# Optimization experiments

Hardware: AMD Instinct MI355X
Metric: run time of the kernel (lower is better)

The kernel has to match this reference:

```python
import jax, jax.numpy as jnp
import numpy as np

N_GRAPHS = 64

def setup_inputs() -> dict:
    key = jax.random.key(0)
    ks = jax.random.split(key, 8)
    N, E, H = 50000, 600000, 128
    x = jax.random.normal(ks[0], (N, 2), dtype=jnp.float32)
    edge_index = jax.random.randint(ks[1], (2, E), 0, N, dtype=jnp.int64)
    batch = jnp.sort(jax.random.randint(ks[2], (N,), 0, N_GRAPHS, dtype=jnp.int64))
    s = 0.1  # keep tanh out of saturation
    return {
        'x': x,
        'edge_index': edge_index,
        'batch': batch,
        'W1': jax.random.normal(ks[3], (2, H), dtype=jnp.float32) * s,
        'b1': jnp.zeros((H,), jnp.float32),
        'W2': jax.random.normal(ks[4], (H, H), dtype=jnp.float32) * s,
        'b2': jnp.zeros((H,), jnp.float32),
        'W3': jax.random.normal(ks[5], (H, H), dtype=jnp.float32) * s,
        'b3': jnp.zeros((H,), jnp.float32),
        'Wo': jax.random.normal(ks[6], (2 * H, 41), dtype=jnp.float32) * s,
        'bo': jnp.zeros((41,), jnp.float32),
    }

def reference(x, edge_index, batch, W1, b1, W2, b2, W3, b3, Wo, bo):
    N = x.shape[0]
    src, dst = edge_index[0], edge_index[1]
    # GCN symmetric normalization with self loops: deg = in-degree + 1
    ones_e = jnp.ones(src.shape[0], dtype=x.dtype)
    deg = jax.ops.segment_sum(ones_e, dst, num_segments=N) + 1.0
    dinv = jax.lax.rsqrt(deg)                       # [N]
    edge_norm = (dinv[src] * dinv[dst])[:, None]    # [E,1]
    self_norm = (dinv * dinv)[:, None]              # [N,1]

    def gcn(h, W, b):
        h = h @ W                                   # [N,H] transform first
        agg = jax.ops.segment_sum(h[src] * edge_norm, dst, num_segments=N)
        return agg + h * self_norm + b

    h = jnp.tanh(gcn(x, W1, b1))
    h = jnp.tanh(gcn(h, W2, b2))
    h = jnp.tanh(gcn(h, W3, b3))

    # global max pool + global mean pool over graphs
    cnt = jax.ops.segment_sum(jnp.ones(N, dtype=h.dtype), batch, num_segments=N_GRAPHS)
    mx = jax.ops.segment_max(h, batch, num_segments=N_GRAPHS)
    mx = jnp.where(cnt[:, None] > 0, mx, 0.0)
    mean = jax.ops.segment_sum(h, batch, num_segments=N_GRAPHS) / jnp.maximum(cnt, 1.0)[:, None]
    pooled = jnp.concatenate([mx, mean], axis=1)    # [G, 2H]
    return jnp.tanh(pooled @ Wo + bo)               # [G, 41]
```

## Files before the change

### kernel.cpp

```cpp
#include <hip/hip_runtime.h>
#include <math.h>

#define NGRAPH 64
#define POOL_CHUNKS 32
#define SCAN_BLK 1024

typedef short short8 __attribute__((ext_vector_type(8)));
typedef float floatx4 __attribute__((ext_vector_type(4)));

__device__ inline unsigned pack_bf16x2(float a, float b) {
    unsigned ua = __float_as_uint(a);
    unsigned ub = __float_as_uint(b);
    ua = (ua + 0x7fffu + ((ua >> 16) & 1u)) >> 16;
    ub = (ub + 0x7fffu + ((ub >> 16) & 1u)) >> 16;
    return ua | (ub << 16);
}
__device__ inline unsigned short bf16_1(float a) {
    unsigned ua = __float_as_uint(a);
    return (unsigned short)((ua + 0x7fffu + ((ua >> 16) & 1u)) >> 16);
}
__device__ inline float bf16lo(unsigned u) { return __uint_as_float(u << 16); }
__device__ inline float bf16hi(unsigned u) { return __uint_as_float(u & 0xffff0000u); }



__global__ void pack_count(const int* __restrict__ dst, int E, int* __restrict__ cnt,
                           const float* __restrict__ W2, const float* __restrict__ W3,
                           unsigned* __restrict__ Wt2, unsigned* __restrict__ Wt3) {
    if (blockIdx.x < 32) {
        int b = blockIdx.x;
        const float* W = (b < 16) ? W2 : W3;
        unsigned* Wt = (b < 16) ? Wt2 : Wt3;
        b &= 15;
        int bk = b & 3, bn = b >> 2;
        __shared__ float s[32][33];
        int tx = threadIdx.x & 31, ty = threadIdx.x >> 5;
#pragma unroll
        for (int r = 0; r < 4; ++r)
            s[r * 8 + ty][tx] = W[(bk * 32 + r * 8 + ty) * 128 + bn * 32 + tx];
        __syncthreads();
        int t16 = threadIdx.x & 15, tn = threadIdx.x >> 4;
#pragma unroll
        for (int pass = 0; pass < 2; ++pass) {
            int nl = pass * 16 + tn;
            unsigned pk = pack_bf16x2(s[2 * t16][nl], s[2 * t16 + 1][nl]);
            Wt[(bn * 32 + nl) * 64 + bk * 16 + t16] = pk;
        }
    } else {
        int e = (blockIdx.x - 32) * blockDim.x + threadIdx.x;
        if (e < E) atomicAdd(&cnt[dst[e]], 1);
    }
}


__global__ __launch_bounds__(SCAN_BLK) void scan_phase1(const int* __restrict__ cnt,
                                                        const float* __restrict__ x,
                                                        int* __restrict__ row_ptr,
                                                        int* __restrict__ bsum,
                                                        float* __restrict__ dinv,
                                                        float2* __restrict__ y, int N) {
    __shared__ int sm[SCAN_BLK];
    int i = blockIdx.x * SCAN_BLK + threadIdx.x;
    int v = (i < N) ? cnt[i] : 0;
    if (i < N) {
        float dv = rsqrtf((float)v + 1.0f);
        dinv[i] = dv;
        float2 xv = ((const float2*)x)[i];
        y[i] = make_float2(xv.x * dv, xv.y * dv);
    }
    sm[threadIdx.x] = v;
    __syncthreads();
    for (int off = 1; off < SCAN_BLK; off <<= 1) {
        int t = (threadIdx.x >= (unsigned)off) ? sm[threadIdx.x - off] : 0;
        __syncthreads();
        sm[threadIdx.x] += t;
        __syncthreads();
    }
    if (i < N) row_ptr[i] = sm[threadIdx.x] - v;
    if (threadIdx.x == SCAN_BLK - 1) bsum[blockIdx.x] = sm[SCAN_BLK - 1];
}

__global__ __launch_bounds__(SCAN_BLK) void scan_phase2(int* __restrict__ bsum, int nb,
                                                        const int* __restrict__ batch, int N,
                                                        int* __restrict__ goff) {
    if (threadIdx.x <= NGRAPH) {
        int g = threadIdx.x;
        int lo = 0, hi = N;
        while (lo < hi) {
            int mid = (lo + hi) >> 1;
            if (batch[mid] < g) lo = mid + 1; else hi = mid;
        }
        goff[g] = lo;
    }
    __shared__ int sm[SCAN_BLK];
    int v = (threadIdx.x < (unsigned)nb) ? bsum[threadIdx.x] : 0;
    sm[threadIdx.x] = v;
    __syncthreads();
    for (int off = 1; off < SCAN_BLK; off <<= 1) {
        int t = (threadIdx.x >= (unsigned)off) ? sm[threadIdx.x - off] : 0;
        __syncthreads();
        sm[threadIdx.x] += t;
        __syncthreads();
    }
    if (threadIdx.x < (unsigned)nb) bsum[threadIdx.x] = sm[threadIdx.x] - v;
}

__global__ __launch_bounds__(SCAN_BLK) void scan_phase3(int* __restrict__ row_ptr,
                                                        const int* __restrict__ bsum,
                                                        int N, int E) {
    int i = blockIdx.x * SCAN_BLK + threadIdx.x;
    if (i < N) row_ptr[i] += bsum[blockIdx.x];
    if (i == 0) row_ptr[N] = E;
}

__global__ void fill_kernel(const int* __restrict__ src, const int* __restrict__ dst, int E,
                            const int* __restrict__ row_ptr, int* __restrict__ cnt,
                            int* __restrict__ col) {
    int e = blockIdx.x * blockDim.x + threadIdx.x;
    if (e < E) {
        int d = dst[e];
        int p = row_ptr[d] + atomicSub(&cnt[d], 1) - 1;
        col[p] = src[e];
    }
}


__global__ __launch_bounds__(256) void agg_x_t1(const float2* __restrict__ y,
                                                const int* __restrict__ row_ptr,
                                                const int* __restrict__ col,
                                                const float* __restrict__ dinv,
                                                const float* __restrict__ W1,
                                                const float* __restrict__ b1,
                                                unsigned short* __restrict__ h, int N) {
    __shared__ float4 sW[64];
    __shared__ float4 sb[32];
    __shared__ float2 zs[256];
    if (threadIdx.x < 64) sW[threadIdx.x] = ((const float4*)W1)[threadIdx.x];
    if (threadIdx.x < 32) sb[threadIdx.x] = ((const float4*)b1)[threadIdx.x];

    int v = blockIdx.x * 256 + threadIdx.x;
    float2 zv = make_float2(0.f, 0.f);
    if (v < N) {
        int s = row_ptr[v], e = row_ptr[v + 1];
        float2 a0 = y[v];
        float2 a1 = make_float2(0.f, 0.f);
        float2 a2 = make_float2(0.f, 0.f);
        float2 a3 = make_float2(0.f, 0.f);
        int j = s;
        for (; j + 4 <= e; j += 4) {
            int u0 = col[j], u1 = col[j + 1], u2 = col[j + 2], u3 = col[j + 3];
            float2 v0 = y[u0], v1 = y[u1], v2 = y[u2], v3 = y[u3];
            a0.x += v0.x; a0.y += v0.y;
            a1.x += v1.x; a1.y += v1.y;
            a2.x += v2.x; a2.y += v2.y;
            a3.x += v3.x; a3.y += v3.y;
        }
        for (; j < e; ++j) {
            float2 vv = y[col[j]];
            a0.x += vv.x; a0.y += vv.y;
        }
        float dv = dinv[v];
        zv = make_float2(dv * (a0.x + a1.x + a2.x + a3.x),
                         dv * (a0.y + a1.y + a2.y + a3.y));
    }
    zs[threadIdx.x] = zv;
    __syncthreads();

    int q = threadIdx.x & 31;
    int rsub = threadIdx.x >> 5;
    float4 w0 = sW[q];
    float4 w1 = sW[32 + q];
    float4 b = sb[q];
    size_t qoff = (size_t)(q >> 3) * N;
#pragma unroll 4
    for (int pass = 0; pass < 32; ++pass) {
        int local = pass * 8 + rsub;
        int row = blockIdx.x * 256 + local;
        if (row >= N) break;
        float2 z = zs[local];
        float ox = tanhf(fmaf(z.x, w0.x, fmaf(z.y, w1.x, b.x)));
        float oy = tanhf(fmaf(z.x, w0.y, fmaf(z.y, w1.y, b.y)));
        float oz = tanhf(fmaf(z.x, w0.z, fmaf(z.y, w1.z, b.z)));
        float ow = tanhf(fmaf(z.x, w0.w, fmaf(z.y, w1.w, b.w)));
        uint2 pk;
        pk.x = pack_bf16x2(ox, oy);
        pk.y = pack_bf16x2(oz, ow);
        ((uint2*)h)[(qoff + row) * 8 + (q & 7)] = pk;
    }
}


__global__ __launch_bounds__(256) void gemm_mfma(const unsigned short* __restrict__ A,
                                                 const unsigned* __restrict__ Wt,
                                                 const float* __restrict__ dinv,
                                                 unsigned short* __restrict__ t, int N) {
    __shared__ unsigned sW[128 * 68];
    const uint4* Wt4 = (const uint4*)Wt;
    for (int i = threadIdx.x; i < 2048; i += 256) {
        int n = i >> 4, c = i & 15;
        *(uint4*)&sW[n * 68 + c * 4] = Wt4[i];
    }
    __syncthreads();
    int w = threadIdx.x >> 6;
    int l = threadIdx.x & 63;
    int lm = l & 15;
    int q4 = l >> 4;
    int k8 = q4 * 8;

    floatx4 acc[2][8];
#pragma unroll
    for (int i = 0; i < 2; ++i)
#pragma unroll
        for (int j = 0; j < 8; ++j) acc[i][j] = (floatx4){0.f, 0.f, 0.f, 0.f};

    int rowbase = blockIdx.x * 128 + w * 32;
#pragma unroll
    for (int ks = 0; ks < 4; ++ks) {
        short8 a[2];
#pragma unroll
        for (int mt = 0; mt < 2; ++mt) {
            int r = min(rowbase + mt * 16 + lm, N - 1);
            a[mt] = *(const short8*)(A + ((size_t)ks * N + r) * 32 + k8);
        }
#pragma unroll
        for (int nt = 0; nt < 8; ++nt) {
            short8 b = *(const short8*)&sW[(nt * 16 + lm) * 68 + ks * 16 + q4 * 4];
#pragma unroll
            for (int mt = 0; mt < 2; ++mt)
                acc[mt][nt] = __builtin_amdgcn_mfma_f32_16x16x32_bf16(a[mt], b, acc[mt][nt], 0, 0, 0);
        }
    }

#pragma unroll
    for (int mt = 0; mt < 2; ++mt) {
#pragma unroll
        for (int reg = 0; reg < 4; ++reg) {
            int gr = rowbase + mt * 16 + q4 * 4 + reg;
            if (gr >= N) continue;
            float dv = dinv[gr];
#pragma unroll
            for (int nt = 0; nt < 8; ++nt) {
                t[((size_t)(nt >> 1) * N + gr) * 32 + (nt & 1) * 16 + lm] =
                    bf16_1(acc[mt][nt][reg] * dv);
            }
        }
    }
}


__global__ __launch_bounds__(256) void agg_kernel(const unsigned short* __restrict__ t,
                                                  const int* __restrict__ row_ptr,
                                                  const int* __restrict__ col,
                                                  const float* __restrict__ dinv,
                                                  const float* __restrict__ bias,
                                                  unsigned short* __restrict__ out, int N) {
    int lane = threadIdx.x & 63;
    int wave = threadIdx.x >> 6;
    int grp = lane >> 2;
    int q = lane & 3;
    int qt = blockIdx.y;
    int node = blockIdx.x * 64 + wave * 16 + grp;
    if (node >= N) return;
    const uint4* t4 = (const uint4*)t;
    unsigned qb = (unsigned)qt * (unsigned)N;
    int s = row_ptr[node];
    int deg = row_ptr[node + 1] - s;

    float a[8];
    {
        uint4 v = t4[(size_t)((qb + (unsigned)node) * 4u + q)];
        a[0] = bf16lo(v.x); a[1] = bf16hi(v.x);
        a[2] = bf16lo(v.y); a[3] = bf16hi(v.y);
        a[4] = bf16lo(v.z); a[5] = bf16hi(v.z);
        a[6] = bf16lo(v.w); a[7] = bf16hi(v.w);
    }
    int j = 0;
    for (; j + 4 <= deg; j += 4) {
        int u0 = col[s + j];
        int u1 = col[s + j + 1];
        int u2 = col[s + j + 2];
        int u3 = col[s + j + 3];
        uint4 v0 = t4[(size_t)((qb + (unsigned)u0) * 4u + q)];
        uint4 v1 = t4[(size_t)((qb + (unsigned)u1) * 4u + q)];
        uint4 v2 = t4[(size_t)((qb + (unsigned)u2) * 4u + q)];
        uint4 v3 = t4[(size_t)((qb + (unsigned)u3) * 4u + q)];
        a[0] += bf16lo(v0.x); a[1] += bf16hi(v0.x);
        a[2] += bf16lo(v0.y); a[3] += bf16hi(v0.y);
        a[4] += bf16lo(v0.z); a[5] += bf16hi(v0.z);
        a[6] += bf16lo(v0.w); a[7] += bf16hi(v0.w);
        a[0] += bf16lo(v1.x); a[1] += bf16hi(v1.x);
        a[2] += bf16lo(v1.y); a[3] += bf16hi(v1.y);
        a[4] += bf16lo(v1.z); a[5] += bf16hi(v1.z);
        a[6] += bf16lo(v1.w); a[7] += bf16hi(v1.w);
        a[0] += bf16lo(v2.x); a[1] += bf16hi(v2.x);
        a[2] += bf16lo(v2.y); a[3] += bf16hi(v2.y);
        a[4] += bf16lo(v2.z); a[5] += bf16hi(v2.z);
        a[6] += bf16lo(v2.w); a[7] += bf16hi(v2.w);
        a[0] += bf16lo(v3.x); a[1] += bf16hi(v3.x);
        a[2] += bf16lo(v3.y); a[3] += bf16hi(v3.y);
        a[4] += bf16lo(v3.z); a[5] += bf16hi(v3.z);
        a[6] += bf16lo(v3.w); a[7] += bf16hi(v3.w);
    }
    for (; j < deg; ++j) {
        int u = col[s + j];
        uint4 v = t4[(size_t)((qb + (unsigned)u) * 4u + q)];
        a[0] += bf16lo(v.x); a[1] += bf16hi(v.x);
        a[2] += bf16lo(v.y); a[3] += bf16hi(v.y);
        a[4] += bf16lo(v.z); a[5] += bf16hi(v.z);
        a[6] += bf16lo(v.w); a[7] += bf16hi(v.w);
    }

    float dv = dinv[node];
    const float4* b4 = (const float4*)bias;
    float4 b0 = b4[qt * 8 + q * 2];
    float4 b1 = b4[qt * 8 + q * 2 + 1];
    uint4 pk;
    pk.x = pack_bf16x2(tanhf(fmaf(dv, a[0], b0.x)), tanhf(fmaf(dv, a[1], b0.y)));
    pk.y = pack_bf16x2(tanhf(fmaf(dv, a[2], b0.z)), tanhf(fmaf(dv, a[3], b0.w)));
    pk.z = pack_bf16x2(tanhf(fmaf(dv, a[4], b1.x)), tanhf(fmaf(dv, a[5], b1.y)));
    pk.w = pack_bf16x2(tanhf(fmaf(dv, a[6], b1.z)), tanhf(fmaf(dv, a[7], b1.w)));
    ((uint4*)out)[(size_t)((qb + (unsigned)node) * 4u + q)] = pk;
}


__global__ __launch_bounds__(128) void pool_partial(const unsigned short* __restrict__ h,
                                                    const int* __restrict__ goff,
                                                    float* __restrict__ part, int N) {
    int g = blockIdx.x;
    int c = blockIdx.y;
    int j = threadIdx.x;
    int s = goff[g], e = goff[g + 1];
    int cnt = e - s;
    int per = (cnt + POOL_CHUNKS - 1) / POOL_CHUNKS;
    int ps = s + c * per;
    int pe = min(ps + per, e);
    size_t qoff = (size_t)(j >> 5) * N;
    int jq = j & 31;
    float mx = -3.402823466e+38f, sm = 0.f;
    for (int n = ps; n < pe; ++n) {
        float v = __uint_as_float(((unsigned)h[(qoff + n) * 32 + jq]) << 16);
        mx = fmaxf(mx, v);
        sm += v;
    }
    float* dst = part + ((size_t)g * POOL_CHUNKS + c) * 256;
    dst[j] = mx;
    dst[128 + j] = sm;
}

__global__ __launch_bounds__(128) void pool_final(const float* __restrict__ part,
                                                  const int* __restrict__ goff,
                                                  const float* __restrict__ Wo,
                                                  const float* __restrict__ bo,
                                                  float* __restrict__ out) {
    __shared__ float p[256];
    int g = blockIdx.x;
    int j = threadIdx.x;
    float mx = -3.402823466e+38f, sm = 0.f;
    const float* base = part + (size_t)g * POOL_CHUNKS * 256;
#pragma unroll 4
    for (int c = 0; c < POOL_CHUNKS; ++c) {
        mx = fmaxf(mx, base[c * 256 + j]);
        sm += base[c * 256 + 128 + j];
    }
    int cnt = goff[g + 1] - goff[g];
    p[j] = (cnt > 0) ? mx : 0.f;
    p[128 + j] = sm / fmaxf((float)cnt, 1.f);
    __syncthreads();
    if (j < 41) {
        float acc = bo[j];
        for (int k = 0; k < 256; ++k) acc = fmaf(p[k], Wo[k * 41 + j], acc);
        out[g * 41 + j] = tanhf(acc);
    }
}


extern "C" void kernel_launch(void* const* d_in, const int* in_sizes, int n_in,
                              void* d_out, int out_size, void* d_ws, size_t ws_size,
                              hipStream_t stream) {
    const float* x   = (const float*)d_in[0];
    const int*   ei  = (const int*)d_in[1];
    const int* batch = (const int*)d_in[2];
    const float* W1  = (const float*)d_in[3];
    const float* b1  = (const float*)d_in[4];
    const float* W2  = (const float*)d_in[5];
    const float* b2  = (const float*)d_in[6];
    const float* W3  = (const float*)d_in[7];
    const float* b3  = (const float*)d_in[8];
    const float* Wo  = (const float*)d_in[9];
    const float* bo  = (const float*)d_in[10];
    float* outp = (float*)d_out;

    int N = in_sizes[2];
    int E = in_sizes[1] / 2;
    const int* src = ei;
    const int* dst = ei + E;

    char* p = (char*)d_ws;
    auto alloc = [&](size_t bytes) -> char* {
        char* q = p;
        p += (bytes + 255) & ~(size_t)255;
        return q;
    };
    unsigned short* t   = (unsigned short*)alloc((size_t)N * 128 * 2);
    unsigned short* hb  = (unsigned short*)alloc((size_t)N * 128 * 2);
    unsigned short* h3b = (unsigned short*)alloc((size_t)N * 128 * 2);
    float* dinv   = (float*)alloc((size_t)N * 4);
    int*   cnt    = (int*)alloc((size_t)N * 4);
    int*   rowp   = (int*)alloc((size_t)(N + 1) * 4);
    int*   col    = (int*)alloc((size_t)E * 4);
    int*   goff   = (int*)alloc(65 * 4);
    float* part   = (float*)alloc((size_t)NGRAPH * POOL_CHUNKS * 256 * 4);
    float2* y     = (float2*)alloc((size_t)N * 8);
    unsigned* Wt2 = (unsigned*)alloc(128 * 64 * 4);
    unsigned* Wt3 = (unsigned*)alloc(128 * 64 * 4);
    int nscan = (N + SCAN_BLK - 1) / SCAN_BLK;
    int*   bsum   = (int*)alloc((size_t)nscan * 4);

    hipMemsetAsync(cnt, 0, (size_t)N * 4, stream);

    pack_count<<<32 + (E + 255) / 256, 256, 0, stream>>>(dst, E, cnt, W2, W3, Wt2, Wt3);
    scan_phase1<<<nscan, SCAN_BLK, 0, stream>>>(cnt, x, rowp, bsum, dinv, y, N);
    scan_phase2<<<1, SCAN_BLK, 0, stream>>>(bsum, nscan, batch, N, goff);
    scan_phase3<<<nscan, SCAN_BLK, 0, stream>>>(rowp, bsum, N, E);
    fill_kernel<<<(E + 255) / 256, 256, 0, stream>>>(src, dst, E, rowp, cnt, col);

    dim3 agrid((N + 63) / 64, 4);

    agg_x_t1<<<(N + 255) / 256, 256, 0, stream>>>(y, rowp, col, dinv, W1, b1, hb, N);
    gemm_mfma<<<(N + 127) / 128, 256, 0, stream>>>(hb, Wt2, dinv, t, N);
    agg_kernel<<<agrid, 256, 0, stream>>>(t, rowp, col, dinv, b2, hb, N);
    gemm_mfma<<<(N + 127) / 128, 256, 0, stream>>>(hb, Wt3, dinv, t, N);
    agg_kernel<<<agrid, 256, 0, stream>>>(t, rowp, col, dinv, b3, h3b, N);

    dim3 pgrid(NGRAPH, POOL_CHUNKS);
    pool_partial<<<pgrid, 128, 0, stream>>>(h3b, goff, part, N);
    pool_final<<<NGRAPH, 128, 0, stream>>>(part, goff, Wo, bo, outp);
}
```

Baseline: 277.9 us.

## Fuse scan phases via last-block ticket and fuse pooling into final aggregation

```diff
diff --git a/kernel.cpp b/kernel.cpp
--- a/kernel.cpp
+++ b/kernel.cpp
@@ -2,7 +2,6 @@
 #include <math.h>
 
 #define NGRAPH 64
-#define POOL_CHUNKS 32
 #define SCAN_BLK 1024
 
 typedef short short8 __attribute__((ext_vector_type(8)));
@@ -21,6 +20,11 @@
 }
 __device__ inline float bf16lo(unsigned u) { return __uint_as_float(u << 16); }
 __device__ inline float bf16hi(unsigned u) { return __uint_as_float(u & 0xffff0000u); }
+
+__device__ inline unsigned fkey(float v) {
+    unsigned u = __float_as_uint(v);
+    return (v >= 0.f) ? (u | 0x80000000u) : ~u;
+}
 
 
 
@@ -53,13 +57,17 @@
 }
 
 
-__global__ __launch_bounds__(SCAN_BLK) void scan_phase1(const int* __restrict__ cnt,
-                                                        const float* __restrict__ x,
-                                                        int* __restrict__ row_ptr,
-                                                        int* __restrict__ bsum,
-                                                        float* __restrict__ dinv,
-                                                        float2* __restrict__ y, int N) {
+__global__ __launch_bounds__(SCAN_BLK) void scanA(const int* __restrict__ cnt,
+                                                  const float* __restrict__ x,
+                                                  int* __restrict__ row_ptr,
+                                                  int* __restrict__ bsum,
+                                                  float* __restrict__ dinv,
+                                                  float2* __restrict__ y,
+                                                  const int* __restrict__ batch,
+                                                  int* __restrict__ ticket,
+                                                  int* __restrict__ goff, int N) {
     __shared__ int sm[SCAN_BLK];
+    __shared__ int amLast;
     int i = blockIdx.x * SCAN_BLK + threadIdx.x;
     int v = (i < N) ? cnt[i] : 0;
     if (i < N) {
@@ -78,11 +86,24 @@
     }
     if (i < N) row_ptr[i] = sm[threadIdx.x] - v;
     if (threadIdx.x == SCAN_BLK - 1) bsum[blockIdx.x] = sm[SCAN_BLK - 1];
-}
-
-__global__ __launch_bounds__(SCAN_BLK) void scan_phase2(int* __restrict__ bsum, int nb,
-                                                        const int* __restrict__ batch, int N,
-                                                        int* __restrict__ goff) {
+    __syncthreads();
+    if (threadIdx.x == 0) {
+        __threadfence();
+        amLast = (atomicAdd(ticket, 1) == (int)gridDim.x - 1);
+    }
+    __syncthreads();
+    if (!amLast) return;
+    int nb = (int)gridDim.x;
+    int v2 = (threadIdx.x < (unsigned)nb) ? atomicAdd(&bsum[threadIdx.x], 0) : 0;
+    sm[threadIdx.x] = v2;
+    __syncthreads();
+    for (int off = 1; off < SCAN_BLK; off <<= 1) {
+        int t = (threadIdx.x >= (unsigned)off) ? sm[threadIdx.x - off] : 0;
+        __syncthreads();
+        sm[threadIdx.x] += t;
+        __syncthreads();
+    }
+    if (threadIdx.x < (unsigned)nb) bsum[threadIdx.x] = sm[threadIdx.x] - v2;
     if (threadIdx.x <= NGRAPH) {
         int g = threadIdx.x;
         int lo = 0, hi = N;
@@ -92,34 +113,16 @@
         }
         goff[g] = lo;
     }
-    __shared__ int sm[SCAN_BLK];
-    int v = (threadIdx.x < (unsigned)nb) ? bsum[threadIdx.x] : 0;
-    sm[threadIdx.x] = v;
-    __syncthreads();
-    for (int off = 1; off < SCAN_BLK; off <<= 1) {
-        int t = (threadIdx.x >= (unsigned)off) ? sm[threadIdx.x - off] : 0;
-        __syncthreads();
-        sm[threadIdx.x] += t;
-        __syncthreads();
-    }
-    if (threadIdx.x < (unsigned)nb) bsum[threadIdx.x] = sm[threadIdx.x] - v;
-}
-
-__global__ __launch_bounds__(SCAN_BLK) void scan_phase3(int* __restrict__ row_ptr,
-                                                        const int* __restrict__ bsum,
-                                                        int N, int E) {
-    int i = blockIdx.x * SCAN_BLK + threadIdx.x;
-    if (i < N) row_ptr[i] += bsum[blockIdx.x];
-    if (i == 0) row_ptr[N] = E;
 }
 
 __global__ void fill_kernel(const int* __restrict__ src, const int* __restrict__ dst, int E,
-                            const int* __restrict__ row_ptr, int* __restrict__ cnt,
-                            int* __restrict__ col) {
+                            const int* __restrict__ row_ptr, const int* __restrict__ bsum,
+                            int* __restrict__ cnt, int* __restrict__ col) {
     int e = blockIdx.x * blockDim.x + threadIdx.x;
     if (e < E) {
         int d = dst[e];
-        int p = row_ptr[d] + atomicSub(&cnt[d], 1) - 1;
+        int base = row_ptr[d] + bsum[d >> 10];
+        int p = base + atomicSub(&cnt[d], 1) - 1;
         col[p] = src[e];
     }
 }
@@ -127,11 +130,12 @@
 
 __global__ __launch_bounds__(256) void agg_x_t1(const float2* __restrict__ y,
                                                 const int* __restrict__ row_ptr,
+                                                const int* __restrict__ bsum,
                                                 const int* __restrict__ col,
                                                 const float* __restrict__ dinv,
                                                 const float* __restrict__ W1,
                                                 const float* __restrict__ b1,
-                                                unsigned short* __restrict__ h, int N) {
+                                                unsigned short* __restrict__ h, int N, int E) {
     __shared__ float4 sW[64];
     __shared__ float4 sb[32];
     __shared__ float2 zs[256];
@@ -141,7 +145,8 @@
     int v = blockIdx.x * 256 + threadIdx.x;
     float2 zv = make_float2(0.f, 0.f);
     if (v < N) {
-        int s = row_ptr[v], e = row_ptr[v + 1];
+        int s = row_ptr[v] + bsum[v >> 10];
+        int e = (v + 1 < N) ? row_ptr[v + 1] + bsum[(v + 1) >> 10] : E;
         float2 a0 = y[v];
         float2 a1 = make_float2(0.f, 0.f);
         float2 a2 = make_float2(0.f, 0.f);
@@ -248,23 +253,22 @@
 }
 
 
-__global__ __launch_bounds__(256) void agg_kernel(const unsigned short* __restrict__ t,
-                                                  const int* __restrict__ row_ptr,
-                                                  const int* __restrict__ col,
-                                                  const float* __restrict__ dinv,
-                                                  const float* __restrict__ bias,
-                                                  unsigned short* __restrict__ out, int N) {
-    int lane = threadIdx.x & 63;
-    int wave = threadIdx.x >> 6;
-    int grp = lane >> 2;
-    int q = lane & 3;
+__global__ __launch_bounds__(1024) void agg_kernel(const unsigned short* __restrict__ t,
+                                                   const int* __restrict__ row_ptr,
+                                                   const int* __restrict__ bsum,
+                                                   const int* __restrict__ col,
+                                                   const float* __restrict__ dinv,
+                                                   const float* __restrict__ bias,
+                                                   unsigned short* __restrict__ out, int N, int E) {
+    int q = threadIdx.x & 3;
+    int node = blockIdx.x * 256 + (threadIdx.x >> 2);
     int qt = blockIdx.y;
-    int node = blockIdx.x * 64 + wave * 16 + grp;
     if (node >= N) return;
     const uint4* t4 = (const uint4*)t;
     unsigned qb = (unsigned)qt * (unsigned)N;
-    int s = row_ptr[node];
-    int deg = row_ptr[node + 1] - s;
+    int s = row_ptr[node] + bsum[node >> 10];
+    int e = (node + 1 < N) ? row_ptr[node + 1] + bsum[(node + 1) >> 10] : E;
+    int deg = e - s;
 
     float a[8];
     {
@@ -323,31 +327,158 @@
 }
 
 
-__global__ __launch_bounds__(128) void pool_partial(const unsigned short* __restrict__ h,
-                                                    const int* __restrict__ goff,
-                                                    float* __restrict__ part, int N) {
-    int g = blockIdx.x;
-    int c = blockIdx.y;
-    int j = threadIdx.x;
-    int s = goff[g], e = goff[g + 1];
-    int cnt = e - s;
-    int per = (cnt + POOL_CHUNKS - 1) / POOL_CHUNKS;
-    int ps = s + c * per;
-    int pe = min(ps + per, e);
-    size_t qoff = (size_t)(j >> 5) * N;
-    int jq = j & 31;
-    float mx = -3.402823466e+38f, sm = 0.f;
-    for (int n = ps; n < pe; ++n) {
-        float v = __uint_as_float(((unsigned)h[(qoff + n) * 32 + jq]) << 16);
-        mx = fmaxf(mx, v);
-        sm += v;
-    }
-    float* dst = part + ((size_t)g * POOL_CHUNKS + c) * 256;
-    dst[j] = mx;
-    dst[128 + j] = sm;
-}
-
-__global__ __launch_bounds__(128) void pool_final(const float* __restrict__ part,
+__global__ __launch_bounds__(1024) void agg3_pool(const unsigned short* __restrict__ t,
+                                                  const int* __restrict__ row_ptr,
+                                                  const int* __restrict__ bsum,
+                                                  const int* __restrict__ col,
+                                                  const float* __restrict__ dinv,
+                                                  const float* __restrict__ bias,
+                                                  const int* __restrict__ batch,
+                                                  unsigned* __restrict__ pmax,
+                                                  float* __restrict__ psum, int N, int E) {
+    __shared__ unsigned smax[2][32];
+    __shared__ float ssum[2][32];
+    if (threadIdx.x < 64) {
+        smax[threadIdx.x >> 5][threadIdx.x & 31] = 0u;
+        ssum[threadIdx.x >> 5][threadIdx.x & 31] = 0.f;
+    }
+    __syncthreads();
+
+    int q = threadIdx.x & 3;
+    int blockBase = (int)blockIdx.x * 256;
+    int node = blockBase + ((int)threadIdx.x >> 2);
+    int qt = blockIdx.y;
+    bool valid = node < N;
+    int nc = valid ? node : N - 1;
+    const uint4* t4 = (const uint4*)t;
+    unsigned qb = (unsigned)qt * (unsigned)N;
+    int s = row_ptr[nc] + bsum[nc >> 10];
+    int e = (nc + 1 < N) ? row_ptr[nc + 1] + bsum[(nc + 1) >> 10] : E;
+    int deg = valid ? (e - s) : 0;
+
+    float a[8];
+    {
+        uint4 v = t4[(size_t)((qb + (unsigned)nc) * 4u + q)];
+        a[0] = bf16lo(v.x); a[1] = bf16hi(v.x);
+        a[2] = bf16lo(v.y); a[3] = bf16hi(v.y);
+        a[4] = bf16lo(v.z); a[5] = bf16hi(v.z);
+        a[6] = bf16lo(v.w); a[7] = bf16hi(v.w);
+    }
+    int j = 0;
+    for (; j + 4 <= deg; j += 4) {
+        int u0 = col[s + j];
+        int u1 = col[s + j + 1];
+        int u2 = col[s + j + 2];
+        int u3 = col[s + j + 3];
+        uint4 v0 = t4[(size_t)((qb + (unsigned)u0) * 4u + q)];
+        uint4 v1 = t4[(size_t)((qb + (unsigned)u1) * 4u + q)];
+        uint4 v2 = t4[(size_t)((qb + (unsigned)u2) * 4u + q)];
+        uint4 v3 = t4[(size_t)((qb + (unsigned)u3) * 4u + q)];
+        a[0] += bf16lo(v0.x); a[1] += bf16hi(v0.x);
+        a[2] += bf16lo(v0.y); a[3] += bf16hi(v0.y);
+        a[4] += bf16lo(v0.z); a[5] += bf16hi(v0.z);
+        a[6] += bf16lo(v0.w); a[7] += bf16hi(v0.w);
+        a[0] += bf16lo(v1.x); a[1] += bf16hi(v1.x);
+        a[2] += bf16lo(v1.y); a[3] += bf16hi(v1.y);
+        a[4] += bf16lo(v1.z); a[5] += bf16hi(v1.z);
+        a[6] += bf16lo(v1.w); a[7] += bf16hi(v1.w);
+        a[0] += bf16lo(v2.x); a[1] += bf16hi(v2.x);
+        a[2] += bf16lo(v2.y); a[3] += bf16hi(v2.y);
+        a[4] += bf16lo(v2.z); a[5] += bf16hi(v2.z);
+        a[6] += bf16lo(v2.w); a[7] += bf16hi(v2.w);
+        a[0] += bf16lo(v3.x); a[1] += bf16hi(v3.x);
+        a[2] += bf16lo(v3.y); a[3] += bf16hi(v3.y);
+        a[4] += bf16lo(v3.z); a[5] += bf16hi(v3.z);
+        a[6] += bf16lo(v3.w); a[7] += bf16hi(v3.w);
+    }
+    for (; j < deg; ++j) {
+        int u = col[s + j];
+        uint4 v = t4[(size_t)((qb + (unsigned)u) * 4u + q)];
+        a[0] += bf16lo(v.x); a[1] += bf16hi(v.x);
+        a[2] += bf16lo(v.y); a[3] += bf16hi(v.y);
+        a[4] += bf16lo(v.z); a[5] += bf16hi(v.z);
+        a[6] += bf16lo(v.w); a[7] += bf16hi(v.w);
+    }
+
+    float dv = dinv[nc];
+    const float4* b4 = (const float4*)bias;
+    float4 b0 = b4[qt * 8 + q * 2];
+    float4 b1 = b4[qt * 8 + q * 2 + 1];
+    float o[8];
+    o[0] = tanhf(fmaf(dv, a[0], b0.x)); o[1] = tanhf(fmaf(dv, a[1], b0.y));
+    o[2] = tanhf(fmaf(dv, a[2], b0.z)); o[3] = tanhf(fmaf(dv, a[3], b0.w));
+    o[4] = tanhf(fmaf(dv, a[4], b1.x)); o[5] = tanhf(fmaf(dv, a[5], b1.y));
+    o[6] = tanhf(fmaf(dv, a[6], b1.z)); o[7] = tanhf(fmaf(dv, a[7], b1.w));
+
+    int g = batch[nc];
+    int g0 = batch[min(blockBase, N - 1)];
+    int gl = __shfl(g, 0, 64);
+    int gh = __shfl(g, 63, 64);
+
+    if (gl == gh) {
+        float m[8], sv[8];
+#pragma unroll
+        for (int k = 0; k < 8; ++k) {
+            m[k] = valid ? o[k] : -3.402823466e+38f;
+            sv[k] = valid ? o[k] : 0.f;
+        }
+#pragma unroll
+        for (int st = 4; st < 64; st <<= 1) {
+#pragma unroll
+            for (int k = 0; k < 8; ++k) {
+                m[k] = fmaxf(m[k], __shfl_xor(m[k], st, 64));
+                sv[k] += __shfl_xor(sv[k], st, 64);
+            }
+        }
+        if (((threadIdx.x & 63) >> 2) == 0) {
+            int seg = gl - g0;
+            if (seg < 2) {
+#pragma unroll
+                for (int k = 0; k < 8; ++k) {
+                    atomicMax(&smax[seg][q * 8 + k], fkey(m[k]));
+                    atomicAdd(&ssum[seg][q * 8 + k], sv[k]);
+                }
+            } else {
+#pragma unroll
+                for (int k = 0; k < 8; ++k) {
+                    atomicMax(&pmax[gl * 128 + qt * 32 + q * 8 + k], fkey(m[k]));
+                    atomicAdd(&psum[gl * 128 + qt * 32 + q * 8 + k], sv[k]);
+                }
+            }
+        }
+    } else {
+        if (valid) {
+            int seg = g - g0;
+            if (seg < 2) {
+#pragma unroll
+                for (int k = 0; k < 8; ++k) {
+                    atomicMax(&smax[seg][q * 8 + k], fkey(o[k]));
+                    atomicAdd(&ssum[seg][q * 8 + k], o[k]);
+                }
+            } else {
+#pragma unroll
+                for (int k = 0; k < 8; ++k) {
+                    atomicMax(&pmax[g * 128 + qt * 32 + q * 8 + k], fkey(o[k]));
+                    atomicAdd(&psum[g * 128 + qt * 32 + q * 8 + k], o[k]);
+                }
+            }
+        }
+    }
+    __syncthreads();
+    if (threadIdx.x < 64) {
+        int seg = threadIdx.x >> 5, c = threadIdx.x & 31;
+        int g0b = batch[min(blockBase, N - 1)];
+        int gg = g0b + seg;
+        if (gg < NGRAPH) {
+            atomicMax(&pmax[gg * 128 + qt * 32 + c], smax[seg][c]);
+            atomicAdd(&psum[gg * 128 + qt * 32 + c], ssum[seg][c]);
+        }
+    }
+}
+
+
+__global__ __launch_bounds__(128) void pool_final(const unsigned* __restrict__ pmax,
+                                                  const float* __restrict__ psum,
                                                   const int* __restrict__ goff,
                                                   const float* __restrict__ Wo,
                                                   const float* __restrict__ bo,
@@ -355,16 +486,12 @@
     __shared__ float p[256];
     int g = blockIdx.x;
     int j = threadIdx.x;
-    float mx = -3.402823466e+38f, sm = 0.f;
-    const float* base = part + (size_t)g * POOL_CHUNKS * 256;
-#pragma unroll 4
-    for (int c = 0; c < POOL_CHUNKS; ++c) {
-        mx = fmaxf(mx, base[c * 256 + j]);
-        sm += base[c * 256 + 128 + j];
-    }
     int cnt = goff[g + 1] - goff[g];
+    unsigned key = pmax[g * 128 + j];
+    float mx = (key & 0x80000000u) ? __uint_as_float(key ^ 0x80000000u)
+                                   : __uint_as_float(~key);
     p[j] = (cnt > 0) ? mx : 0.f;
-    p[128 + j] = sm / fmaxf((float)cnt, 1.f);
+    p[128 + j] = psum[g * 128 + j] / fmaxf((float)cnt, 1.f);
     __syncthreads();
     if (j < 41) {
         float acc = bo[j];
@@ -403,36 +530,35 @@
     };
     unsigned short* t   = (unsigned short*)alloc((size_t)N * 128 * 2);
     unsigned short* hb  = (unsigned short*)alloc((size_t)N * 128 * 2);
-    unsigned short* h3b = (unsigned short*)alloc((size_t)N * 128 * 2);
     float* dinv   = (float*)alloc((size_t)N * 4);
-    int*   cnt    = (int*)alloc((size_t)N * 4);
     int*   rowp   = (int*)alloc((size_t)(N + 1) * 4);
     int*   col    = (int*)alloc((size_t)E * 4);
     int*   goff   = (int*)alloc(65 * 4);
-    float* part   = (float*)alloc((size_t)NGRAPH * POOL_CHUNKS * 256 * 4);
     float2* y     = (float2*)alloc((size_t)N * 8);
     unsigned* Wt2 = (unsigned*)alloc(128 * 64 * 4);
     unsigned* Wt3 = (unsigned*)alloc(128 * 64 * 4);
     int nscan = (N + SCAN_BLK - 1) / SCAN_BLK;
     int*   bsum   = (int*)alloc((size_t)nscan * 4);
-
-    hipMemsetAsync(cnt, 0, (size_t)N * 4, stream);
+    size_t cntB = ((size_t)N * 4 + 255) & ~(size_t)255;
+    char* zbase = alloc(cntB + 256 + NGRAPH * 128 * 4 * 2);
+    int*      cnt  = (int*)zbase;
+    int*      tick = (int*)(zbase + cntB);
+    unsigned* pmax = (unsigned*)(zbase + cntB + 256);
+    float*    psum = (float*)(zbase + cntB + 256 + NGRAPH * 128 * 4);
+
+    (void)hipMemsetAsync(zbase, 0, cntB + 256 + NGRAPH * 128 * 4 * 2, stream);
 
     pack_count<<<32 + (E + 255) / 256, 256, 0, stream>>>(dst, E, cnt, W2, W3, Wt2, Wt3);
-    scan_phase1<<<nscan, SCAN_BLK, 0, stream>>>(cnt, x, rowp, bsum, dinv, y, N);
-    scan_phase2<<<1, SCAN_BLK, 0, stream>>>(bsum, nscan, batch, N, goff);
-    scan_phase3<<<nscan, SCAN_BLK, 0, stream>>>(rowp, bsum, N, E);
-    fill_kernel<<<(E + 255) / 256, 256, 0, stream>>>(src, dst, E, rowp, cnt, col);
-
-    dim3 agrid((N + 63) / 64, 4);
-
-    agg_x_t1<<<(N + 255) / 256, 256, 0, stream>>>(y, rowp, col, dinv, W1, b1, hb, N);
+    scanA<<<nscan, SCAN_BLK, 0, stream>>>(cnt, x, rowp, bsum, dinv, y, batch, tick, goff, N);
+    fill_kernel<<<(E + 255) / 256, 256, 0, stream>>>(src, dst, E, rowp, bsum, cnt, col);
+
+    dim3 agrid((N + 255) / 256, 4);
+
+    agg_x_t1<<<(N + 255) / 256, 256, 0, stream>>>(y, rowp, bsum, col, dinv, W1, b1, hb, N, E);
     gemm_mfma<<<(N + 127) / 128, 256, 0, stream>>>(hb, Wt2, dinv, t, N);
-    agg_kernel<<<agrid, 256, 0, stream>>>(t, rowp, col, dinv, b2, hb, N);
+    agg_kernel<<<agrid, 1024, 0, stream>>>(t, rowp, bsum, col, dinv, b2, hb, N, E);
     gemm_mfma<<<(N + 127) / 128, 256, 0, stream>>>(hb, Wt3, dinv, t, N);
-    agg_kernel<<<agrid, 256, 0, stream>>>(t, rowp, col, dinv, b3, h3b, N);
-
-    dim3 pgrid(NGRAPH, POOL_CHUNKS);
-    pool_partial<<<pgrid, 128, 0, stream>>>(h3b, goff, part, N);
-    pool_final<<<NGRAPH, 128, 0, stream>>>(part, goff, Wo, bo, outp);
-}
+    agg3_pool<<<agrid, 1024, 0, stream>>>(t, rowp, bsum, col, dinv, b3, batch, pmax, psum, N, E);
+
+    pool_final<<<NGRAPH, 128, 0, stream>>>(pmax, psum, goff, Wo, bo, outp);
+}
```

Measured after the change: 274.6 us. Within noise of the previous version (-1.2%).
